# Kernel optimization log

Hardware: AMD Instinct MI355X
Metric: run time of the kernel (lower is better)

Reference implementation:

```python
import jax, jax.numpy as jnp
import numpy as np

N = 50000
H = 8
D = 32
E = 400000
IN = 128
NEG_SLOPE = 0.2


def _gat(h, edges, W, al, ar, b):
    # DGL GATConv: fc -> per-head attention logits -> edge softmax over dst -> aggregate
    src, dst = edges[0], edges[1]
    feat = (h @ W).reshape(N, H, D)                      # [N,H,D]
    el = jnp.einsum('nhd,hd->nh', feat, al)              # [N,H]
    er = jnp.einsum('nhd,hd->nh', feat, ar)              # [N,H]
    e = jax.nn.leaky_relu(el[src] + er[dst], NEG_SLOPE)  # [E,H]
    m = jax.ops.segment_max(e, dst, num_segments=N)      # [N,H] per-dst max
    m = jnp.where(jnp.isfinite(m), m, 0.0)
    m = jax.lax.stop_gradient(m)
    ex = jnp.exp(e - m[dst])                             # [E,H]
    denom = jax.ops.segment_sum(ex, dst, num_segments=N) # [N,H]
    alpha = ex / denom[dst]                              # edge softmax
    out = jax.ops.segment_sum(feat[src] * alpha[:, :, None], dst, num_segments=N)  # [N,H,D]
    return (out + b.reshape(1, H, D)).reshape(N, H * D)


def setup_inputs() -> dict:
    key = jax.random.key(0)
    ks = jax.random.split(key, 12)
    s = 0.05
    return {
        'h': jax.random.normal(ks[0], (N, IN), jnp.float32),
        'edges0': jax.random.randint(ks[1], (2, E), 0, N, jnp.int32),
        'edges1': jax.random.randint(ks[2], (2, E), 0, N, jnp.int32),
        'fc0': jax.random.normal(ks[3], (IN, H * D), jnp.float32) * s,
        'al0': jax.random.normal(ks[4], (H, D), jnp.float32) * s,
        'ar0': jax.random.normal(ks[5], (H, D), jnp.float32) * s,
        'bias0': jnp.zeros((H * D,), jnp.float32),
        'fc1': jax.random.normal(ks[6], (IN, H * D), jnp.float32) * s,
        'al1': jax.random.normal(ks[7], (H, D), jnp.float32) * s,
        'ar1': jax.random.normal(ks[8], (H, D), jnp.float32) * s,
        'bias1': jnp.zeros((H * D,), jnp.float32),
        'sw1': jax.random.normal(ks[9], (H * D, 128), jnp.float32) * s,
        'sb1': jnp.zeros((128,), jnp.float32),
        'sw2': jax.random.normal(ks[10], (128, 1), jnp.float32) * s,
    }


def reference(h, edges0, edges1, fc0, al0, ar0, bias0, fc1, al1, ar1, bias1, sw1, sb1, sw2):
    z0 = _gat(h, edges0, fc0, al0, ar0, bias0)   # [N, H*D]
    z1 = _gat(h, edges1, fc1, al1, ar1, bias1)   # [N, H*D]
    z = jnp.stack([z0, z1], axis=1)              # [N, M=2, H*D]
    # semantic attention: MLP -> mean over nodes -> softmax over meta-paths
    w = jnp.tanh(z @ sw1 + sb1) @ sw2            # [N,M,1]
    beta = jax.nn.softmax(w.mean(axis=0), axis=0)  # [M,1]
    return (beta[None] * z).sum(axis=1)          # [N, H*D]
```

## Files before the change

### kernel.cpp

```cpp
#include <hip/hip_runtime.h>
#include <math.h>

#define NEG_SLOPE 0.2f

typedef unsigned int uint;
typedef unsigned short ushort;
typedef __bf16 bf16x8 __attribute__((ext_vector_type(8)));
typedef float f32x4 __attribute__((ext_vector_type(4)));

__device__ __forceinline__ uint bf16r(float a) {
    uint u = __float_as_uint(a);
    return (u + 0x7fffu + ((u >> 16) & 1u)) >> 16;
}
__device__ __forceinline__ uint bf16pack(float a, float b) {
    return bf16r(a) | (bf16r(b) << 16);
}
__device__ __forceinline__ float bflo(uint u) { return __uint_as_float(u << 16); }
__device__ __forceinline__ float bfhi(uint u) { return __uint_as_float(u & 0xffff0000u); }

__global__ void prep_kernel(const float* __restrict__ fc0, const float* __restrict__ fc1,
                            const float* __restrict__ sw1, ushort* __restrict__ wbt,
                            ushort* __restrict__ sw1t, float* __restrict__ wsum,
                            int* __restrict__ count, int* __restrict__ cursor, int Ntot) {
    int b = blockIdx.x;
    if (b == 0 && threadIdx.x == 0) { wsum[0] = 0.f; wsum[1] = 0.f; }
    if (b < 256) {
        int idx = b * 256 + threadIdx.x;
        const float* W = (idx >> 15) ? fc1 : fc0;
        int r = idx & 32767;
        int c = r >> 7, k = r & 127;
        wbt[idx] = (ushort)bf16r(W[(size_t)k * 256 + c]);
    } else if (b < 384) {
        int idx = (b - 256) * 256 + threadIdx.x;
        int c = idx >> 8, p = idx & 255;
        int col = (p & ~63) + ((p & 3) * 16) + ((p >> 2) & 15);
        sw1t[idx] = (ushort)bf16r(sw1[(size_t)col * 128 + c]);
    } else {
        int i = (b - 384) * 256 + threadIdx.x;
        if (i < Ntot) { count[i] = 0; cursor[i] = 0; }
    }
}

__global__ void hist_kernel(const int* __restrict__ e0, const int* __restrict__ e1,
                            int* __restrict__ count, int E, int N) {
    int e = blockIdx.x * blockDim.x + threadIdx.x;
    if (e >= 2 * E) return;
    int l = (e >= E);
    int ee = e - l * E;
    const int* edges = l ? e1 : e0;
    atomicAdd(&count[edges[E + ee] + l * N], 1);
}

__global__ void scan1_kernel(const int* __restrict__ count, int* __restrict__ base,
                             int* __restrict__ bsum, int Ntot) {
    __shared__ int ws_s[4];
    int b = blockIdx.x;
    int i = b * 256 + threadIdx.x;
    int v = (i < Ntot) ? count[i] : 0;
    int lane = threadIdx.x & 63;
    int wid = threadIdx.x >> 6;
    int x = v;
#pragma unroll
    for (int s = 1; s < 64; s <<= 1) {
        int y = __shfl_up(x, s, 64);
        if (lane >= s) x += y;
    }
    if (lane == 63) ws_s[wid] = x;
    __syncthreads();
    int add = 0;
    for (int w = 0; w < wid; w++) add += ws_s[w];
    int incl = x + add;
    if (i < Ntot) base[i] = incl - v;
    if (threadIdx.x == 255) bsum[b] = incl;
}

__global__ void scan2_kernel(int* __restrict__ bsum, int nb) {
    __shared__ int ws_s[4];
    __shared__ int running_s;
    if (threadIdx.x == 0) running_s = 0;
    __syncthreads();
    int lane = threadIdx.x & 63;
    int wid = threadIdx.x >> 6;
    for (int c0 = 0; c0 < nb; c0 += 256) {
        int i = c0 + threadIdx.x;
        int v = (i < nb) ? bsum[i] : 0;
        int x = v;
#pragma unroll
        for (int s = 1; s < 64; s <<= 1) {
            int y = __shfl_up(x, s, 64);
            if (lane >= s) x += y;
        }
        if (lane == 63) ws_s[wid] = x;
        __syncthreads();
        int add = 0;
        for (int w = 0; w < wid; w++) add += ws_s[w];
        int incl = x + add;
        int run = running_s;
        if (i < nb) bsum[i] = run + incl - v;
        __syncthreads();
        if (threadIdx.x == 255) running_s = run + incl;
        __syncthreads();
    }
}

#define HKPAD 136
__global__ void __launch_bounds__(256, 4)
fc_kernel(const float* __restrict__ h, const ushort* __restrict__ wbt,
          const float* __restrict__ al0, const float* __restrict__ ar0,
          const float* __restrict__ al1, const float* __restrict__ ar1,
          ushort* __restrict__ featb, float* __restrict__ el,
          float* __restrict__ er, int N, int nb) {
    __shared__ ushort hs[64 * HKPAD];
    int b = blockIdx.x;
    int l = (b >= nb);
    int n0 = (b - l * nb) * 64;
    for (int t = threadIdx.x; t < 64 * 32; t += 256) {
        int r = t >> 5, i4 = t & 31;
        int n = n0 + r;
        float4 v = make_float4(0.f, 0.f, 0.f, 0.f);
        if (n < N) v = ((const float4*)h)[(size_t)n * 32 + i4];
        uint2 pk;
        pk.x = bf16pack(v.x, v.y);
        pk.y = bf16pack(v.z, v.w);
        *((uint2*)(hs + r * HKPAD + i4 * 4)) = pk;
    }
    __syncthreads();

    const ushort* wb = wbt + l * 32768;
    const float* al = l ? al1 : al0;
    const float* ar = l ? ar1 : ar0;
    ushort* fb = featb + (size_t)l * N * 256;
    float* elp = el + (size_t)l * N * 8;
    float* erp = er + (size_t)l * N * 8;

    int wv = threadIdx.x >> 6;
    int lane = threadIdx.x & 63;
    int lhi = lane >> 4, llo = lane & 15;

    f32x4 acc[4][4];
#pragma unroll
    for (int cb = 0; cb < 4; cb++)
#pragma unroll
        for (int rt = 0; rt < 4; rt++) acc[cb][rt] = (f32x4){0.f, 0.f, 0.f, 0.f};

#pragma unroll
    for (int ks = 0; ks < 4; ks++) {
        bf16x8 a[4];
#pragma unroll
        for (int rt = 0; rt < 4; rt++)
            a[rt] = *(const bf16x8*)(hs + (rt * 16 + llo) * HKPAD + ks * 32 + lhi * 8);
#pragma unroll
        for (int cb = 0; cb < 4; cb++) {
            bf16x8 bfrag = *(const bf16x8*)(wb + (size_t)(64 * wv + 16 * cb + llo) * 128 + ks * 32 + lhi * 8);
#pragma unroll
            for (int rt = 0; rt < 4; rt++)
                acc[cb][rt] = __builtin_amdgcn_mfma_f32_16x16x32_bf16(a[rt], bfrag, acc[cb][rt], 0, 0, 0);
        }
    }

    float alv0 = al[64 * wv + llo],      alv1 = al[64 * wv + 16 + llo];
    float alv2 = al[64 * wv + 32 + llo], alv3 = al[64 * wv + 48 + llo];
    float arv0 = ar[64 * wv + llo],      arv1 = ar[64 * wv + 16 + llo];
    float arv2 = ar[64 * wv + 32 + llo], arv3 = ar[64 * wv + 48 + llo];

#pragma unroll
    for (int rt = 0; rt < 4; rt++) {
#pragma unroll
        for (int reg = 0; reg < 4; reg++) {
            int n = n0 + rt * 16 + lhi * 4 + reg;
            bool valid = (n < N);
            uint2 pv;
            pv.x = bf16pack(acc[0][rt][reg], acc[1][rt][reg]);
            pv.y = bf16pack(acc[2][rt][reg], acc[3][rt][reg]);
            if (valid) *((uint2*)(fb + (size_t)n * 256 + 64 * wv + 4 * llo)) = pv;
            float pl0 = acc[0][rt][reg] * alv0 + acc[1][rt][reg] * alv1;
            float pl1 = acc[2][rt][reg] * alv2 + acc[3][rt][reg] * alv3;
            float pr0 = acc[0][rt][reg] * arv0 + acc[1][rt][reg] * arv1;
            float pr1 = acc[2][rt][reg] * arv2 + acc[3][rt][reg] * arv3;
#pragma unroll
            for (int s = 1; s <= 8; s <<= 1) {
                pl0 += __shfl_xor(pl0, s, 64);
                pl1 += __shfl_xor(pl1, s, 64);
                pr0 += __shfl_xor(pr0, s, 64);
                pr1 += __shfl_xor(pr1, s, 64);
            }
            if (llo == 0 && valid) {
                *((float2*)(elp + (size_t)n * 8 + 2 * wv)) = make_float2(pl0, pl1);
                *((float2*)(erp + (size_t)n * 8 + 2 * wv)) = make_float2(pr0, pr1);
            }
        }
    }
}

__global__ void scatter_kernel(const int* __restrict__ e0, const int* __restrict__ e1,
                               const float* __restrict__ el, const float* __restrict__ er,
                               const int* __restrict__ base, const int* __restrict__ bsum,
                               int* __restrict__ cursor, int* __restrict__ csr_src,
                               float* __restrict__ pedge, int E, int N) {
    int e = blockIdx.x * blockDim.x + threadIdx.x;
    if (e >= 2 * E) return;
    int l = (e >= E);
    int ee = e - l * E;
    const int* edges = l ? e1 : e0;
    int src = edges[ee];
    int dst = edges[E + ee];
    int d = dst + l * N;
    int pos = base[d] + bsum[d >> 8] + atomicAdd(&cursor[d], 1);
    csr_src[pos] = src;
    size_t so = (size_t)(l * N + src) * 2;
    size_t dofs = (size_t)(l * N + dst) * 2;
    float4 l0 = ((const float4*)el)[so];
    float4 l1 = ((const float4*)el)[so + 1];
    float4 r0 = ((const float4*)er)[dofs];
    float4 r1 = ((const float4*)er)[dofs + 1];
    float v[8] = {l0.x + r0.x, l0.y + r0.y, l0.z + r0.z, l0.w + r0.w,
                  l1.x + r1.x, l1.y + r1.y, l1.z + r1.z, l1.w + r1.w};
#pragma unroll
    for (int k = 0; k < 8; k++) {
        float t = (v[k] > 0.f) ? v[k] : NEG_SLOPE * v[k];
        v[k] = __expf(t);
    }
    ((float4*)pedge)[pos * 2]     = make_float4(v[0], v[1], v[2], v[3]);
    ((float4*)pedge)[pos * 2 + 1] = make_float4(v[4], v[5], v[6], v[7]);
}

__global__ void aggregate_csr_kernel(const int* __restrict__ csr_src, const float* __restrict__ pedge,
                                     const int* __restrict__ base, const int* __restrict__ bsum,
                                     const int* __restrict__ count, const ushort* __restrict__ featb,
                                     const float* __restrict__ bias0, const float* __restrict__ bias1,
                                     ushort* __restrict__ z0b, ushort* __restrict__ z1b, int N) {
    int wid = threadIdx.x >> 6;
    int lane = threadIdx.x & 63;
    int d = blockIdx.x * 4 + wid;
    if (d >= 2 * N) return;
    int l = (d >= N);
    int dst = d - l * N;
    int row0 = base[d] + bsum[d >> 8];
    int deg = count[d];
    int w = lane >> 4, llo = lane & 15;
    const ushort* fb = featb + (size_t)l * N * 256;
    const float2* pe = (const float2*)(pedge + (size_t)row0 * 8);
    const int* cs = csr_src + row0;
    const uint2* fb2 = (const uint2*)fb;

    float d0 = 0.f, d1 = 0.f;
    float4 a = make_float4(0.f, 0.f, 0.f, 0.f);
    int t = 0;
    for (; t + 4 <= deg; t += 4) {
        int s0 = cs[t], s1 = cs[t + 1], s2 = cs[t + 2], s3 = cs[t + 3];
        float2 q0 = pe[t * 4 + w];
        float2 q1 = pe[t * 4 + 4 + w];
        float2 q2 = pe[t * 4 + 8 + w];
        float2 q3 = pe[t * 4 + 12 + w];
        uint2 u0 = fb2[(size_t)s0 * 64 + lane];
        uint2 u1 = fb2[(size_t)s1 * 64 + lane];
        uint2 u2 = fb2[(size_t)s2 * 64 + lane];
        uint2 u3 = fb2[(size_t)s3 * 64 + lane];
        d0 += q0.x; d1 += q0.y;
        a.x += q0.x * bflo(u0.x); a.y += q0.x * bfhi(u0.x);
        a.z += q0.y * bflo(u0.y); a.w += q0.y * bfhi(u0.y);
        d0 += q1.x; d1 += q1.y;
        a.x += q1.x * bflo(u1.x); a.y += q1.x * bfhi(u1.x);
        a.z += q1.y * bflo(u1.y); a.w += q1.y * bfhi(u1.y);
        d0 += q2.x; d1 += q2.y;
        a.x += q2.x * bflo(u2.x); a.y += q2.x * bfhi(u2.x);
        a.z += q2.y * bflo(u2.y); a.w += q2.y * bfhi(u2.y);
        d0 += q3.x; d1 += q3.y;
        a.x += q3.x * bflo(u3.x); a.y += q3.x * bfhi(u3.x);
        a.z += q3.y * bflo(u3.y); a.w += q3.y * bfhi(u3.y);
    }
    for (; t < deg; t++) {
        int s0 = cs[t];
        float2 q0 = pe[t * 4 + w];
        uint2 u0 = fb2[(size_t)s0 * 64 + lane];
        d0 += q0.x; d1 += q0.y;
        a.x += q0.x * bflo(u0.x); a.y += q0.x * bfhi(u0.x);
        a.z += q0.y * bflo(u0.y); a.w += q0.y * bfhi(u0.y);
    }
    const float* bias = l ? bias1 : bias0;
    int c0 = 64 * w + llo;
    float b0 = bias[c0], b1 = bias[c0 + 16], b2 = bias[c0 + 32], b3 = bias[c0 + 48];
    float i0 = (d0 > 0.f) ? 1.f / d0 : 0.f;
    float i1 = (d1 > 0.f) ? 1.f / d1 : 0.f;
    uint2 o;
    o.x = bf16pack(a.x * i0 + b0, a.y * i0 + b1);
    o.y = bf16pack(a.z * i1 + b2, a.w * i1 + b3);
    ushort* zb = l ? z1b : z0b;
    ((uint2*)zb)[(size_t)dst * 64 + lane] = o;
}

#define ZROW 264
__global__ void __launch_bounds__(256, 4)
semantic_kernel(const ushort* __restrict__ z0b, const ushort* __restrict__ z1b,
                const ushort* __restrict__ sw1t, const float* __restrict__ sb1,
                const float* __restrict__ sw2, float* __restrict__ wsum, int N) {
    __shared__ ushort zs[64 * ZROW];
    __shared__ float rowp[64];
    int n0 = blockIdx.x * 32;
    if (threadIdx.x < 64) rowp[threadIdx.x] = 0.f;
    for (int t = threadIdx.x; t < 64 * 32; t += 256) {
        int row = t >> 5, i16 = t & 31;
        int r = row >> 1, mm = row & 1;
        int n = n0 + r;
        uint4 v = make_uint4(0u, 0u, 0u, 0u);
        if (n < N) v = ((const uint4*)(mm ? z1b : z0b))[(size_t)n * 32 + i16];
        *((uint4*)(zs + row * ZROW + i16 * 8)) = v;
    }
    __syncthreads();

    int wv = threadIdx.x >> 6;
    int lane = threadIdx.x & 63;
    int lhi = lane >> 4, llo = lane & 15;

    f32x4 acc[2][4];
#pragma unroll
    for (int c = 0; c < 2; c++)
#pragma unroll
        for (int rt = 0; rt < 4; rt++) acc[c][rt] = (f32x4){0.f, 0.f, 0.f, 0.f};

#pragma unroll
    for (int ks = 0; ks < 8; ks++) {
        bf16x8 b0 = *(const bf16x8*)(sw1t + (size_t)((2 * wv) * 16 + llo) * 256 + ks * 32 + lhi * 8);
        bf16x8 b1 = *(const bf16x8*)(sw1t + (size_t)((2 * wv + 1) * 16 + llo) * 256 + ks * 32 + lhi * 8);
#pragma unroll
        for (int rt = 0; rt < 4; rt++) {
            bf16x8 av = *(const bf16x8*)(zs + (rt * 16 + llo) * ZROW + ks * 32 + lhi * 8);
            acc[0][rt] = __builtin_amdgcn_mfma_f32_16x16x32_bf16(av, b0, acc[0][rt], 0, 0, 0);
            acc[1][rt] = __builtin_amdgcn_mfma_f32_16x16x32_bf16(av, b1, acc[1][rt], 0, 0, 0);
        }
    }

    float sb0 = sb1[(2 * wv) * 16 + llo],      s20 = sw2[(2 * wv) * 16 + llo];
    float sb1v = sb1[(2 * wv + 1) * 16 + llo], s21 = sw2[(2 * wv + 1) * 16 + llo];
#pragma unroll
    for (int rt = 0; rt < 4; rt++) {
        float pr[4];
#pragma unroll
        for (int reg = 0; reg < 4; reg++)
            pr[reg] = tanhf(acc[0][rt][reg] + sb0) * s20 + tanhf(acc[1][rt][reg] + sb1v) * s21;
#pragma unroll
        for (int s = 1; s <= 8; s <<= 1)
#pragma unroll
            for (int reg = 0; reg < 4; reg++) pr[reg] += __shfl_xor(pr[reg], s, 64);
        if (llo == 0) {
#pragma unroll
            for (int reg = 0; reg < 4; reg++)
                atomicAdd(&rowp[rt * 16 + lhi * 4 + reg], pr[reg]);
        }
    }
    __syncthreads();
    if (threadIdx.x < 64) {
        int node = n0 + (threadIdx.x >> 1);
        float v = (node < N) ? rowp[threadIdx.x] : 0.f;
        v += __shfl_xor(v, 2, 64);
        v += __shfl_xor(v, 4, 64);
        v += __shfl_xor(v, 8, 64);
        v += __shfl_xor(v, 16, 64);
        v += __shfl_xor(v, 32, 64);
        if (threadIdx.x < 2) atomicAdd(&wsum[threadIdx.x], v);
    }
}

__global__ void combine_kernel(float* __restrict__ out, const ushort* __restrict__ z0b,
                               const ushort* __restrict__ z1b, const float* __restrict__ wsum,
                               float invN, int N) {
    int idx = blockIdx.x * 256 + threadIdx.x;
    if (idx >= N * 64) return;
    float w0 = wsum[0] * invN, w1 = wsum[1] * invN;
    float mx = fmaxf(w0, w1);
    float e0 = __expf(w0 - mx), e1 = __expf(w1 - mx);
    float b0 = e0 / (e0 + e1), b1 = e1 / (e0 + e1);
    int n = idx >> 6, lane = idx & 63;
    int w = lane >> 4, llo = lane & 15;
    uint2 a = ((const uint2*)z0b)[idx];
    uint2 b = ((const uint2*)z1b)[idx];
    float* o = out + (size_t)n * 256 + 64 * w + llo;
    o[0]  = b0 * bflo(a.x) + b1 * bflo(b.x);
    o[16] = b0 * bfhi(a.x) + b1 * bfhi(b.x);
    o[32] = b0 * bflo(a.y) + b1 * bflo(b.y);
    o[48] = b0 * bfhi(a.y) + b1 * bfhi(b.y);
}

extern "C" void kernel_launch(void* const* d_in, const int* in_sizes, int n_in,
                              void* d_out, int out_size, void* d_ws, size_t ws_size,
                              hipStream_t stream) {
    const float* h      = (const float*)d_in[0];
    const int*   edges0 = (const int*)d_in[1];
    const int*   edges1 = (const int*)d_in[2];
    const float* fc0    = (const float*)d_in[3];
    const float* al0    = (const float*)d_in[4];
    const float* ar0    = (const float*)d_in[5];
    const float* bias0  = (const float*)d_in[6];
    const float* fc1    = (const float*)d_in[7];
    const float* al1    = (const float*)d_in[8];
    const float* ar1    = (const float*)d_in[9];
    const float* bias1  = (const float*)d_in[10];
    const float* sw1    = (const float*)d_in[11];
    const float* sb1    = (const float*)d_in[12];
    const float* sw2    = (const float*)d_in[13];

    const int N = in_sizes[0] / 128;
    const int E = in_sizes[1] / 2;
    const int Ntot = 2 * N;
    const int NB2 = (Ntot + 255) / 256;
    const int nb = (N + 63) / 64;

    char* ws = (char*)d_ws;
    ushort* featb = (ushort*)ws;
    ushort* z0b   = featb + (size_t)Ntot * 256;
    ushort* z1b   = z0b + (size_t)N * 256;
    ushort* wbt   = z1b + (size_t)N * 256;
    ushort* sw1t  = wbt + 2 * 256 * 128;
    float*  el    = (float*)(sw1t + 128 * 256);
    float*  er    = el + (size_t)Ntot * 8;
    float*  pedge = er + (size_t)Ntot * 8;
    int*    csr_src = (int*)(pedge + (size_t)E * 16);
    int*    count   = csr_src + 2 * E;
    int*    base    = count + Ntot;
    int*    cursor  = base + Ntot;
    int*    bsum    = cursor + Ntot;
    float*  wsum  = (float*)(bsum + NB2 + 2);
    float*  outp  = (float*)d_out;

    prep_kernel<<<384 + NB2, 256, 0, stream>>>(fc0, fc1, sw1, wbt, sw1t, wsum,
                                               count, cursor, Ntot);
    hist_kernel<<<(2 * E + 255) / 256, 256, 0, stream>>>(edges0, edges1, count, E, N);
    scan1_kernel<<<NB2, 256, 0, stream>>>(count, base, bsum, Ntot);
    scan2_kernel<<<1, 256, 0, stream>>>(bsum, NB2);
    fc_kernel<<<2 * nb, 256, 0, stream>>>(h, wbt, al0, ar0, al1, ar1, featb, el, er, N, nb);
    scatter_kernel<<<(2 * E + 255) / 256, 256, 0, stream>>>(edges0, edges1, el, er, base, bsum,
                                                            cursor, csr_src, pedge, E, N);
    aggregate_csr_kernel<<<(Ntot + 3) / 4, 256, 0, stream>>>(csr_src, pedge, base, bsum, count,
                                                             featb, bias0, bias1, z0b, z1b, N);
    semantic_kernel<<<(N + 31) / 32, 256, 0, stream>>>(z0b, z1b, sw1t, sb1, sw2, wsum, N);
    combine_kernel<<<(N * 64 + 255) / 256, 256, 0, stream>>>(outp, z0b, z1b, wsum,
                                                             1.0f / (float)N, N);
}
```

Before: 260.2 us.

## Fuse histogram into FC kernel, share h tile across layers, widen aggregation unroll

Merges the destination-degree histogram into the FC kernel as extra blocks, which removes a launch and lets the atomics overlap the MFMA work. Each FC block now loads its h tile once and computes both meta-path projections from it, halving h reads and conversions. The CSR aggregation loop is unrolled by 8 to put more gathers in flight, and tanhf in the semantic MLP is replaced by an exp/rcp approximation. The costs are more registers per FC block and aggregation thread, and slightly different tanh rounding.

```diff
diff --git a/kernel.cpp b/kernel.cpp
--- a/kernel.cpp
+++ b/kernel.cpp
@@ -17,6 +17,12 @@
 }
 __device__ __forceinline__ float bflo(uint u) { return __uint_as_float(u << 16); }
 __device__ __forceinline__ float bfhi(uint u) { return __uint_as_float(u & 0xffff0000u); }
+
+__device__ __forceinline__ float fast_tanh(float x) {
+    x = fminf(fmaxf(x, -15.f), 15.f);
+    float t = __expf(2.f * x);
+    return 1.f - 2.f * __builtin_amdgcn_rcpf(t + 1.f);
+}
 
 __global__ void prep_kernel(const float* __restrict__ fc0, const float* __restrict__ fc1,
                             const float* __restrict__ sw1, ushort* __restrict__ wbt,
@@ -41,16 +47,6 @@
     }
 }
 
-__global__ void hist_kernel(const int* __restrict__ e0, const int* __restrict__ e1,
-                            int* __restrict__ count, int E, int N) {
-    int e = blockIdx.x * blockDim.x + threadIdx.x;
-    if (e >= 2 * E) return;
-    int l = (e >= E);
-    int ee = e - l * E;
-    const int* edges = l ? e1 : e0;
-    atomicAdd(&count[edges[E + ee] + l * N], 1);
-}
-
 __global__ void scan1_kernel(const int* __restrict__ count, int* __restrict__ base,
                              int* __restrict__ bsum, int Ntot) {
     __shared__ int ws_s[4];
@@ -105,15 +101,26 @@
 
 #define HKPAD 136
 __global__ void __launch_bounds__(256, 4)
-fc_kernel(const float* __restrict__ h, const ushort* __restrict__ wbt,
-          const float* __restrict__ al0, const float* __restrict__ ar0,
-          const float* __restrict__ al1, const float* __restrict__ ar1,
-          ushort* __restrict__ featb, float* __restrict__ el,
-          float* __restrict__ er, int N, int nb) {
+fc_hist_kernel(const float* __restrict__ h, const ushort* __restrict__ wbt,
+               const float* __restrict__ al0, const float* __restrict__ ar0,
+               const float* __restrict__ al1, const float* __restrict__ ar1,
+               ushort* __restrict__ featb, float* __restrict__ el,
+               float* __restrict__ er, int N, int nb_fc,
+               const int* __restrict__ e0, const int* __restrict__ e1,
+               int* __restrict__ count, int E) {
     __shared__ ushort hs[64 * HKPAD];
     int b = blockIdx.x;
-    int l = (b >= nb);
-    int n0 = (b - l * nb) * 64;
+    if (b >= nb_fc) {
+        int e = (b - nb_fc) * 256 + threadIdx.x;
+        if (e < 2 * E) {
+            int l = (e >= E);
+            int ee = e - l * E;
+            const int* edges = l ? e1 : e0;
+            atomicAdd(&count[edges[E + ee] + l * N], 1);
+        }
+        return;
+    }
+    int n0 = b * 64;
     for (int t = threadIdx.x; t < 64 * 32; t += 256) {
         int r = t >> 5, i4 = t & 31;
         int n = n0 + r;
@@ -126,67 +133,69 @@
     }
     __syncthreads();
 
-    const ushort* wb = wbt + l * 32768;
-    const float* al = l ? al1 : al0;
-    const float* ar = l ? ar1 : ar0;
-    ushort* fb = featb + (size_t)l * N * 256;
-    float* elp = el + (size_t)l * N * 8;
-    float* erp = er + (size_t)l * N * 8;
-
     int wv = threadIdx.x >> 6;
     int lane = threadIdx.x & 63;
     int lhi = lane >> 4, llo = lane & 15;
 
-    f32x4 acc[4][4];
-#pragma unroll
-    for (int cb = 0; cb < 4; cb++)
-#pragma unroll
-        for (int rt = 0; rt < 4; rt++) acc[cb][rt] = (f32x4){0.f, 0.f, 0.f, 0.f};
-
-#pragma unroll
-    for (int ks = 0; ks < 4; ks++) {
-        bf16x8 a[4];
-#pragma unroll
-        for (int rt = 0; rt < 4; rt++)
-            a[rt] = *(const bf16x8*)(hs + (rt * 16 + llo) * HKPAD + ks * 32 + lhi * 8);
-#pragma unroll
-        for (int cb = 0; cb < 4; cb++) {
-            bf16x8 bfrag = *(const bf16x8*)(wb + (size_t)(64 * wv + 16 * cb + llo) * 128 + ks * 32 + lhi * 8);
+    for (int l = 0; l < 2; l++) {
+        const ushort* wb = wbt + l * 32768;
+        const float* al = l ? al1 : al0;
+        const float* ar = l ? ar1 : ar0;
+        ushort* fb = featb + (size_t)l * N * 256;
+        float* elp = el + (size_t)l * N * 8;
+        float* erp = er + (size_t)l * N * 8;
+
+        f32x4 acc[4][4];
+#pragma unroll
+        for (int cb = 0; cb < 4; cb++)
+#pragma unroll
+            for (int rt = 0; rt < 4; rt++) acc[cb][rt] = (f32x4){0.f, 0.f, 0.f, 0.f};
+
+#pragma unroll
+        for (int ks = 0; ks < 4; ks++) {
+            bf16x8 a[4];
 #pragma unroll
             for (int rt = 0; rt < 4; rt++)
-                acc[cb][rt] = __builtin_amdgcn_mfma_f32_16x16x32_bf16(a[rt], bfrag, acc[cb][rt], 0, 0, 0);
-        }
-    }
-
-    float alv0 = al[64 * wv + llo],      alv1 = al[64 * wv + 16 + llo];
-    float alv2 = al[64 * wv + 32 + llo], alv3 = al[64 * wv + 48 + llo];
-    float arv0 = ar[64 * wv + llo],      arv1 = ar[64 * wv + 16 + llo];
-    float arv2 = ar[64 * wv + 32 + llo], arv3 = ar[64 * wv + 48 + llo];
-
-#pragma unroll
-    for (int rt = 0; rt < 4; rt++) {
-#pragma unroll
-        for (int reg = 0; reg < 4; reg++) {
-            int n = n0 + rt * 16 + lhi * 4 + reg;
-            bool valid = (n < N);
-            uint2 pv;
-            pv.x = bf16pack(acc[0][rt][reg], acc[1][rt][reg]);
-            pv.y = bf16pack(acc[2][rt][reg], acc[3][rt][reg]);
-            if (valid) *((uint2*)(fb + (size_t)n * 256 + 64 * wv + 4 * llo)) = pv;
-            float pl0 = acc[0][rt][reg] * alv0 + acc[1][rt][reg] * alv1;
-            float pl1 = acc[2][rt][reg] * alv2 + acc[3][rt][reg] * alv3;
-            float pr0 = acc[0][rt][reg] * arv0 + acc[1][rt][reg] * arv1;
-            float pr1 = acc[2][rt][reg] * arv2 + acc[3][rt][reg] * arv3;
-#pragma unroll
-            for (int s = 1; s <= 8; s <<= 1) {
-                pl0 += __shfl_xor(pl0, s, 64);
-                pl1 += __shfl_xor(pl1, s, 64);
-                pr0 += __shfl_xor(pr0, s, 64);
-                pr1 += __shfl_xor(pr1, s, 64);
+                a[rt] = *(const bf16x8*)(hs + (rt * 16 + llo) * HKPAD + ks * 32 + lhi * 8);
+#pragma unroll
+            for (int cb = 0; cb < 4; cb++) {
+                bf16x8 bfrag = *(const bf16x8*)(wb + (size_t)(64 * wv + 16 * cb + llo) * 128 + ks * 32 + lhi * 8);
+#pragma unroll
+                for (int rt = 0; rt < 4; rt++)
+                    acc[cb][rt] = __builtin_amdgcn_mfma_f32_16x16x32_bf16(a[rt], bfrag, acc[cb][rt], 0, 0, 0);
             }
-            if (llo == 0 && valid) {
-                *((float2*)(elp + (size_t)n * 8 + 2 * wv)) = make_float2(pl0, pl1);
-                *((float2*)(erp + (size_t)n * 8 + 2 * wv)) = make_float2(pr0, pr1);
+        }
+
+        float alv0 = al[64 * wv + llo],      alv1 = al[64 * wv + 16 + llo];
+        float alv2 = al[64 * wv + 32 + llo], alv3 = al[64 * wv + 48 + llo];
+        float arv0 = ar[64 * wv + llo],      arv1 = ar[64 * wv + 16 + llo];
+        float arv2 = ar[64 * wv + 32 + llo], arv3 = ar[64 * wv + 48 + llo];
+
+#pragma unroll
+        for (int rt = 0; rt < 4; rt++) {
+#pragma unroll
+            for (int reg = 0; reg < 4; reg++) {
+                int n = n0 + rt * 16 + lhi * 4 + reg;
+                bool valid = (n < N);
+                uint2 pv;
+                pv.x = bf16pack(acc[0][rt][reg], acc[1][rt][reg]);
+                pv.y = bf16pack(acc[2][rt][reg], acc[3][rt][reg]);
+                if (valid) *((uint2*)(fb + (size_t)n * 256 + 64 * wv + 4 * llo)) = pv;
+                float pl0 = acc[0][rt][reg] * alv0 + acc[1][rt][reg] * alv1;
+                float pl1 = acc[2][rt][reg] * alv2 + acc[3][rt][reg] * alv3;
+                float pr0 = acc[0][rt][reg] * arv0 + acc[1][rt][reg] * arv1;
+                float pr1 = acc[2][rt][reg] * arv2 + acc[3][rt][reg] * arv3;
+#pragma unroll
+                for (int s = 1; s <= 8; s <<= 1) {
+                    pl0 += __shfl_xor(pl0, s, 64);
+                    pl1 += __shfl_xor(pl1, s, 64);
+                    pr0 += __shfl_xor(pr0, s, 64);
+                    pr1 += __shfl_xor(pr1, s, 64);
+                }
+                if (llo == 0 && valid) {
+                    *((float2*)(elp + (size_t)n * 8 + 2 * wv)) = make_float2(pl0, pl1);
+                    *((float2*)(erp + (size_t)n * 8 + 2 * wv)) = make_float2(pr0, pr1);
+                }
             }
         }
     }
@@ -224,6 +233,11 @@
     ((float4*)pedge)[pos * 2 + 1] = make_float4(v[4], v[5], v[6], v[7]);
 }
 
+#define AGG_STEP(qq, uu)                                        \
+    d0 += (qq).x; d1 += (qq).y;                                 \
+    a.x += (qq).x * bflo((uu).x); a.y += (qq).x * bfhi((uu).x); \
+    a.z += (qq).y * bflo((uu).y); a.w += (qq).y * bfhi((uu).y);
+
 __global__ void aggregate_csr_kernel(const int* __restrict__ csr_src, const float* __restrict__ pedge,
                                      const int* __restrict__ base, const int* __restrict__ bsum,
                                      const int* __restrict__ count, const ushort* __restrict__ featb,
@@ -238,44 +252,44 @@
     int row0 = base[d] + bsum[d >> 8];
     int deg = count[d];
     int w = lane >> 4, llo = lane & 15;
-    const ushort* fb = featb + (size_t)l * N * 256;
     const float2* pe = (const float2*)(pedge + (size_t)row0 * 8);
     const int* cs = csr_src + row0;
-    const uint2* fb2 = (const uint2*)fb;
+    const uint2* fb2 = (const uint2*)(featb + (size_t)l * N * 256);
 
     float d0 = 0.f, d1 = 0.f;
     float4 a = make_float4(0.f, 0.f, 0.f, 0.f);
     int t = 0;
+    for (; t + 8 <= deg; t += 8) {
+        int s[8];
+#pragma unroll
+        for (int j = 0; j < 8; j++) s[j] = cs[t + j];
+        float2 q[8];
+#pragma unroll
+        for (int j = 0; j < 8; j++) q[j] = pe[(t + j) * 4 + w];
+        uint2 u[8];
+#pragma unroll
+        for (int j = 0; j < 8; j++) u[j] = fb2[(size_t)s[j] * 64 + lane];
+#pragma unroll
+        for (int j = 0; j < 8; j++) { AGG_STEP(q[j], u[j]) }
+    }
     for (; t + 4 <= deg; t += 4) {
-        int s0 = cs[t], s1 = cs[t + 1], s2 = cs[t + 2], s3 = cs[t + 3];
-        float2 q0 = pe[t * 4 + w];
-        float2 q1 = pe[t * 4 + 4 + w];
-        float2 q2 = pe[t * 4 + 8 + w];
-        float2 q3 = pe[t * 4 + 12 + w];
-        uint2 u0 = fb2[(size_t)s0 * 64 + lane];
-        uint2 u1 = fb2[(size_t)s1 * 64 + lane];
-        uint2 u2 = fb2[(size_t)s2 * 64 + lane];
-        uint2 u3 = fb2[(size_t)s3 * 64 + lane];
-        d0 += q0.x; d1 += q0.y;
-        a.x += q0.x * bflo(u0.x); a.y += q0.x * bfhi(u0.x);
-        a.z += q0.y * bflo(u0.y); a.w += q0.y * bfhi(u0.y);
-        d0 += q1.x; d1 += q1.y;
-        a.x += q1.x * bflo(u1.x); a.y += q1.x * bfhi(u1.x);
-        a.z += q1.y * bflo(u1.y); a.w += q1.y * bfhi(u1.y);
-        d0 += q2.x; d1 += q2.y;
-        a.x += q2.x * bflo(u2.x); a.y += q2.x * bfhi(u2.x);
-        a.z += q2.y * bflo(u2.y); a.w += q2.y * bfhi(u2.y);
-        d0 += q3.x; d1 += q3.y;
-        a.x += q3.x * bflo(u3.x); a.y += q3.x * bfhi(u3.x);
-        a.z += q3.y * bflo(u3.y); a.w += q3.y * bfhi(u3.y);
+        int s[4];
+#pragma unroll
+        for (int j = 0; j < 4; j++) s[j] = cs[t + j];
+        float2 q[4];
+#pragma unroll
+        for (int j = 0; j < 4; j++) q[j] = pe[(t + j) * 4 + w];
+        uint2 u[4];
+#pragma unroll
+        for (int j = 0; j < 4; j++) u[j] = fb2[(size_t)s[j] * 64 + lane];
+#pragma unroll
+        for (int j = 0; j < 4; j++) { AGG_STEP(q[j], u[j]) }
     }
     for (; t < deg; t++) {
         int s0 = cs[t];
         float2 q0 = pe[t * 4 + w];
         uint2 u0 = fb2[(size_t)s0 * 64 + lane];
-        d0 += q0.x; d1 += q0.y;
-        a.x += q0.x * bflo(u0.x); a.y += q0.x * bfhi(u0.x);
-        a.z += q0.y * bflo(u0.y); a.w += q0.y * bfhi(u0.y);
+        AGG_STEP(q0, u0)
     }
     const float* bias = l ? bias1 : bias0;
     int c0 = 64 * w + llo;
@@ -337,7 +351,7 @@
         float pr[4];
 #pragma unroll
         for (int reg = 0; reg < 4; reg++)
-            pr[reg] = tanhf(acc[0][rt][reg] + sb0) * s20 + tanhf(acc[1][rt][reg] + sb1v) * s21;
+            pr[reg] = fast_tanh(acc[0][rt][reg] + sb0) * s20 + fast_tanh(acc[1][rt][reg] + sb1v) * s21;
 #pragma unroll
         for (int s = 1; s <= 8; s <<= 1)
 #pragma unroll
@@ -403,7 +417,8 @@
     const int E = in_sizes[1] / 2;
     const int Ntot = 2 * N;
     const int NB2 = (Ntot + 255) / 256;
-    const int nb = (N + 63) / 64;
+    const int nb_fc = (N + 63) / 64;
+    const int nb_hist = (2 * E + 255) / 256;
 
     char* ws = (char*)d_ws;
     ushort* featb = (ushort*)ws;
@@ -424,10 +439,11 @@
 
     prep_kernel<<<384 + NB2, 256, 0, stream>>>(fc0, fc1, sw1, wbt, sw1t, wsum,
                                                count, cursor, Ntot);
-    hist_kernel<<<(2 * E + 255) / 256, 256, 0, stream>>>(edges0, edges1, count, E, N);
+    fc_hist_kernel<<<nb_fc + nb_hist, 256, 0, stream>>>(h, wbt, al0, ar0, al1, ar1,
+                                                        featb, el, er, N, nb_fc,
+                                                        edges0, edges1, count, E);
     scan1_kernel<<<NB2, 256, 0, stream>>>(count, base, bsum, Ntot);
     scan2_kernel<<<1, 256, 0, stream>>>(bsum, NB2);
-    fc_kernel<<<2 * nb, 256, 0, stream>>>(h, wbt, al0, ar0, al1, ar1, featb, el, er, N, nb);
     scatter_kernel<<<(2 * E + 255) / 256, 256, 0, stream>>>(edges0, edges1, el, er, base, bsum,
                                                             cursor, csr_src, pedge, E, N);
     aggregate_csr_kernel<<<(Ntot + 3) / 4, 256, 0, stream>>>(csr_src, pedge, base, bsum, count,
```

After: 300.7 us. +15.6%, slower.

## Replace two-pass CSR scan with atomic per-wave row allocation; use fast tanh

Applied to the files above, without the earlier changes.

The two-kernel prefix scan (block scan plus single-block scan of block sums) is replaced with one kernel where each wave scans its counts and reserves a contiguous range through an atomicAdd on a global cursor. The CSR rows are no longer in node order but stay contiguous per destination, which is all the scatter and aggregate kernels need. This saves a kernel launch and the serial single-block pass, and scatter/aggregate read one offset array instead of two. The semantic MLP also swaps tanhf for an exp-and-reciprocal approximation, which is cheaper but slightly less accurate.

```diff
diff --git a/kernel.cpp b/kernel.cpp
--- a/kernel.cpp
+++ b/kernel.cpp
@@ -18,12 +18,20 @@
 __device__ __forceinline__ float bflo(uint u) { return __uint_as_float(u << 16); }
 __device__ __forceinline__ float bfhi(uint u) { return __uint_as_float(u & 0xffff0000u); }
 
+__device__ __forceinline__ float fast_tanh(float x) {
+    x = fminf(fmaxf(x, -15.f), 15.f);
+    float t = __expf(2.f * x);
+    return 1.f - 2.f * __builtin_amdgcn_rcpf(t + 1.f);
+}
+
 __global__ void prep_kernel(const float* __restrict__ fc0, const float* __restrict__ fc1,
                             const float* __restrict__ sw1, ushort* __restrict__ wbt,
                             ushort* __restrict__ sw1t, float* __restrict__ wsum,
+                            int* __restrict__ gcur,
                             int* __restrict__ count, int* __restrict__ cursor, int Ntot) {
     int b = blockIdx.x;
     if (b == 0 && threadIdx.x == 0) { wsum[0] = 0.f; wsum[1] = 0.f; }
+    if (b == 0 && threadIdx.x == 1) { *gcur = 0; }
     if (b < 256) {
         int idx = b * 256 + threadIdx.x;
         const float* W = (idx >> 15) ? fc1 : fc0;
@@ -51,56 +59,22 @@
     atomicAdd(&count[edges[E + ee] + l * N], 1);
 }
 
-__global__ void scan1_kernel(const int* __restrict__ count, int* __restrict__ base,
-                             int* __restrict__ bsum, int Ntot) {
-    __shared__ int ws_s[4];
-    int b = blockIdx.x;
-    int i = b * 256 + threadIdx.x;
+__global__ void alloc_kernel(const int* __restrict__ count, int* __restrict__ row0,
+                             int* __restrict__ gcur, int Ntot) {
+    int i = blockIdx.x * 256 + threadIdx.x;
     int v = (i < Ntot) ? count[i] : 0;
     int lane = threadIdx.x & 63;
-    int wid = threadIdx.x >> 6;
     int x = v;
 #pragma unroll
     for (int s = 1; s < 64; s <<= 1) {
         int y = __shfl_up(x, s, 64);
         if (lane >= s) x += y;
     }
-    if (lane == 63) ws_s[wid] = x;
-    __syncthreads();
-    int add = 0;
-    for (int w = 0; w < wid; w++) add += ws_s[w];
-    int incl = x + add;
-    if (i < Ntot) base[i] = incl - v;
-    if (threadIdx.x == 255) bsum[b] = incl;
-}
-
-__global__ void scan2_kernel(int* __restrict__ bsum, int nb) {
-    __shared__ int ws_s[4];
-    __shared__ int running_s;
-    if (threadIdx.x == 0) running_s = 0;
-    __syncthreads();
-    int lane = threadIdx.x & 63;
-    int wid = threadIdx.x >> 6;
-    for (int c0 = 0; c0 < nb; c0 += 256) {
-        int i = c0 + threadIdx.x;
-        int v = (i < nb) ? bsum[i] : 0;
-        int x = v;
-#pragma unroll
-        for (int s = 1; s < 64; s <<= 1) {
-            int y = __shfl_up(x, s, 64);
-            if (lane >= s) x += y;
-        }
-        if (lane == 63) ws_s[wid] = x;
-        __syncthreads();
-        int add = 0;
-        for (int w = 0; w < wid; w++) add += ws_s[w];
-        int incl = x + add;
-        int run = running_s;
-        if (i < nb) bsum[i] = run + incl - v;
-        __syncthreads();
-        if (threadIdx.x == 255) running_s = run + incl;
-        __syncthreads();
-    }
+    int wtot = __shfl(x, 63, 64);
+    int wbase = 0;
+    if (lane == 0) wbase = atomicAdd(gcur, wtot);
+    wbase = __shfl(wbase, 0, 64);
+    if (i < Ntot) row0[i] = wbase + x - v;
 }
 
 #define HKPAD 136
@@ -194,9 +168,9 @@
 
 __global__ void scatter_kernel(const int* __restrict__ e0, const int* __restrict__ e1,
                                const float* __restrict__ el, const float* __restrict__ er,
-                               const int* __restrict__ base, const int* __restrict__ bsum,
-                               int* __restrict__ cursor, int* __restrict__ csr_src,
-                               float* __restrict__ pedge, int E, int N) {
+                               const int* __restrict__ row0, int* __restrict__ cursor,
+                               int* __restrict__ csr_src, float* __restrict__ pedge,
+                               int E, int N) {
     int e = blockIdx.x * blockDim.x + threadIdx.x;
     if (e >= 2 * E) return;
     int l = (e >= E);
@@ -205,7 +179,7 @@
     int src = edges[ee];
     int dst = edges[E + ee];
     int d = dst + l * N;
-    int pos = base[d] + bsum[d >> 8] + atomicAdd(&cursor[d], 1);
+    int pos = row0[d] + atomicAdd(&cursor[d], 1);
     csr_src[pos] = src;
     size_t so = (size_t)(l * N + src) * 2;
     size_t dofs = (size_t)(l * N + dst) * 2;
@@ -225,8 +199,8 @@
 }
 
 __global__ void aggregate_csr_kernel(const int* __restrict__ csr_src, const float* __restrict__ pedge,
-                                     const int* __restrict__ base, const int* __restrict__ bsum,
-                                     const int* __restrict__ count, const ushort* __restrict__ featb,
+                                     const int* __restrict__ row0arr, const int* __restrict__ count,
+                                     const ushort* __restrict__ featb,
                                      const float* __restrict__ bias0, const float* __restrict__ bias1,
                                      ushort* __restrict__ z0b, ushort* __restrict__ z1b, int N) {
     int wid = threadIdx.x >> 6;
@@ -235,13 +209,12 @@
     if (d >= 2 * N) return;
     int l = (d >= N);
     int dst = d - l * N;
-    int row0 = base[d] + bsum[d >> 8];
+    int row0 = row0arr[d];
     int deg = count[d];
     int w = lane >> 4, llo = lane & 15;
-    const ushort* fb = featb + (size_t)l * N * 256;
     const float2* pe = (const float2*)(pedge + (size_t)row0 * 8);
     const int* cs = csr_src + row0;
-    const uint2* fb2 = (const uint2*)fb;
+    const uint2* fb2 = (const uint2*)(featb + (size_t)l * N * 256);
 
     float d0 = 0.f, d1 = 0.f;
     float4 a = make_float4(0.f, 0.f, 0.f, 0.f);
@@ -337,7 +310,7 @@
         float pr[4];
 #pragma unroll
         for (int reg = 0; reg < 4; reg++)
-            pr[reg] = tanhf(acc[0][rt][reg] + sb0) * s20 + tanhf(acc[1][rt][reg] + sb1v) * s21;
+            pr[reg] = fast_tanh(acc[0][rt][reg] + sb0) * s20 + fast_tanh(acc[1][rt][reg] + sb1v) * s21;
 #pragma unroll
         for (int s = 1; s <= 8; s <<= 1)
 #pragma unroll
@@ -416,21 +389,20 @@
     float*  pedge = er + (size_t)Ntot * 8;
     int*    csr_src = (int*)(pedge + (size_t)E * 16);
     int*    count   = csr_src + 2 * E;
-    int*    base    = count + Ntot;
-    int*    cursor  = base + Ntot;
-    int*    bsum    = cursor + Ntot;
-    float*  wsum  = (float*)(bsum + NB2 + 2);
+    int*    row0    = count + Ntot;
+    int*    cursor  = row0 + Ntot;
+    int*    gcur    = cursor + Ntot;
+    float*  wsum  = (float*)(gcur + 1);
     float*  outp  = (float*)d_out;
 
-    prep_kernel<<<384 + NB2, 256, 0, stream>>>(fc0, fc1, sw1, wbt, sw1t, wsum,
+    prep_kernel<<<384 + NB2, 256, 0, stream>>>(fc0, fc1, sw1, wbt, sw1t, wsum, gcur,
                                                count, cursor, Ntot);
     hist_kernel<<<(2 * E + 255) / 256, 256, 0, stream>>>(edges0, edges1, count, E, N);
-    scan1_kernel<<<NB2, 256, 0, stream>>>(count, base, bsum, Ntot);
-    scan2_kernel<<<1, 256, 0, stream>>>(bsum, NB2);
+    alloc_kernel<<<NB2, 256, 0, stream>>>(count, row0, gcur, Ntot);
     fc_kernel<<<2 * nb, 256, 0, stream>>>(h, wbt, al0, ar0, al1, ar1, featb, el, er, N, nb);
-    scatter_kernel<<<(2 * E + 255) / 256, 256, 0, stream>>>(edges0, edges1, el, er, base, bsum,
+    scatter_kernel<<<(2 * E + 255) / 256, 256, 0, stream>>>(edges0, edges1, el, er, row0,
                                                             cursor, csr_src, pedge, E, N);
-    aggregate_csr_kernel<<<(Ntot + 3) / 4, 256, 0, stream>>>(csr_src, pedge, base, bsum, count,
+    aggregate_csr_kernel<<<(Ntot + 3) / 4, 256, 0, stream>>>(csr_src, pedge, row0, count,
                                                              featb, bias0, bias1, z0b, z1b, N);
     semantic_kernel<<<(N + 31) / 32, 256, 0, stream>>>(z0b, z1b, sw1t, sb1, sw2, wsum, N);
     combine_kernel<<<(N * 64 + 255) / 256, 256, 0, stream>>>(outp, z0b, z1b, wsum,
```

New measurement: 270.6 us. +4.0%, slower.
